# Kernel optimization log

Measured on AMD Instinct MI355X. Metric: run time of the kernel, lower is better.

The kernel has to match this reference:

```python
import jax, jax.numpy as jnp
import numpy as np

N_NODES = 100000
N_EDGES = 1600000
IN_DIM = 32
OUT_DIM = 64


def setup_inputs() -> dict:
    key = jax.random.key(0)
    k1, k2, k3, k4, k5 = jax.random.split(key, 5)
    feature = jax.random.normal(k1, (N_NODES, IN_DIM), dtype=jnp.float32)
    src = jax.random.randint(k2, (N_EDGES,), 0, N_NODES, dtype=jnp.int32)
    dst = jax.random.randint(k3, (N_EDGES,), 0, N_NODES, dtype=jnp.int32)
    W = jax.random.normal(k4, (IN_DIM, OUT_DIM), dtype=jnp.float32) * (1.0 / np.sqrt(IN_DIM))
    b = jax.random.normal(k5, (OUT_DIM,), dtype=jnp.float32) * 0.01
    return {"feature": feature, "src": src, "dst": dst, "W": W, "b": b}


def reference(feature, src, dst, W, b):
    # copy_u + sum: gather source features along edges, segment-sum into dst nodes
    msgs = feature[src]  # [E, in_dim]
    h_neigh = jax.ops.segment_sum(msgs, dst, num_segments=N_NODES)  # [N, in_dim]
    # linear projection
    return h_neigh @ W + b  # [N, out_dim]
```

## Files before the change

### kernel.cpp

```cpp
#include <hip/hip_runtime.h>

#define IN_DIM 32
#define OUT_DIM 64
#define NB_SCAN 391

__global__ __launch_bounds__(256) void hist_kernel(
    const int* __restrict__ dst, int* __restrict__ counts, int n_edges) {
    int e = blockIdx.x * 256 + threadIdx.x;
    if (e < n_edges) atomicAdd(&counts[dst[e]], 1);
}

__global__ __launch_bounds__(256) void scan1_kernel(
    const int* __restrict__ counts, int* __restrict__ row_start,
    int* __restrict__ block_sums, int n) {
    __shared__ int tmp[256];
    int tx = threadIdx.x;
    int idx = blockIdx.x * 256 + tx;
    int v = (idx < n) ? counts[idx] : 0;
    tmp[tx] = v;
    __syncthreads();
    for (int off = 1; off < 256; off <<= 1) {
        int t = (tx >= off) ? tmp[tx - off] : 0;
        __syncthreads();
        tmp[tx] += t;
        __syncthreads();
    }
    if (idx < n) row_start[idx] = tmp[tx] - v;
    if (tx == 255) block_sums[blockIdx.x] = tmp[255];
}

__global__ __launch_bounds__(512) void scan2_kernel(int* __restrict__ block_sums, int nb) {
    __shared__ int tmp[512];
    int tx = threadIdx.x;
    int v = (tx < nb) ? block_sums[tx] : 0;
    tmp[tx] = v;
    __syncthreads();
    for (int off = 1; off < 512; off <<= 1) {
        int t = (tx >= off) ? tmp[tx - off] : 0;
        __syncthreads();
        tmp[tx] += t;
        __syncthreads();
    }
    if (tx < nb) block_sums[tx] = tmp[tx] - v;
}

__global__ __launch_bounds__(256) void finalize_kernel(
    int* __restrict__ row_start, const int* __restrict__ block_sums,
    int* __restrict__ cursor, int n, int n_edges) {
    int idx = blockIdx.x * 256 + threadIdx.x;
    if (idx < n) {
        int v = row_start[idx] + block_sums[blockIdx.x];
        row_start[idx] = v;
        cursor[idx] = v;
    }
    if (blockIdx.x == 0 && threadIdx.x == 0) row_start[n] = n_edges;
}

__global__ __launch_bounds__(256) void scatter_kernel(
    const int* __restrict__ src, const int* __restrict__ dst,
    int* __restrict__ cursor, int* __restrict__ edge_src, int n_edges) {
    int e = blockIdx.x * 256 + threadIdx.x;
    if (e < n_edges) {
        int pos = atomicAdd(&cursor[dst[e]], 1);
        edge_src[pos] = src[e];
    }
}

__global__ __launch_bounds__(256) void gather_proj_kernel(
    const float* __restrict__ feature, const int* __restrict__ row_start,
    const int* __restrict__ edge_src, const float* __restrict__ W,
    const float* __restrict__ b, float* __restrict__ out, int n_nodes) {
    __shared__ float Ws[IN_DIM * OUT_DIM];
    __shared__ float bs[OUT_DIM];
    __shared__ float hs[8][IN_DIM];
    int tx = threadIdx.x;

    for (int i = tx; i < IN_DIM * OUT_DIM; i += 256) Ws[i] = W[i];
    if (tx < OUT_DIM) bs[tx] = b[tx];

    int slot = tx >> 5, lane = tx & 31;
    int node = blockIdx.x * 8 + slot;
    float acc = 0.0f;
    if (node < n_nodes) {
        int s0 = row_start[node], s1 = row_start[node + 1];
        int i = s0;
        for (; i + 4 <= s1; i += 4) {
            int ea = edge_src[i], eb = edge_src[i + 1];
            int ec = edge_src[i + 2], ed = edge_src[i + 3];
            float fa = feature[(long long)ea * IN_DIM + lane];
            float fb = feature[(long long)eb * IN_DIM + lane];
            float fc = feature[(long long)ec * IN_DIM + lane];
            float fd = feature[(long long)ed * IN_DIM + lane];
            acc += fa + fb + fc + fd;
        }
        for (; i < s1; ++i) acc += feature[(long long)edge_src[i] * IN_DIM + lane];
    }
    hs[slot][lane] = acc;
    __syncthreads();

    int node0 = blockIdx.x * 8;
#pragma unroll
    for (int it = 0; it < 2; ++it) {
        int idx = tx + it * 256;
        int sl = idx >> 6, col = idx & 63;
        int n2 = node0 + sl;
        if (n2 >= n_nodes) continue;
        float a = bs[col];
#pragma unroll
        for (int k = 0; k < IN_DIM; ++k) a += hs[sl][k] * Ws[k * OUT_DIM + col];
        out[(long long)n2 * OUT_DIM + col] = a;
    }
}

extern "C" void kernel_launch(void* const* d_in, const int* in_sizes, int n_in,
                              void* d_out, int out_size, void* d_ws, size_t ws_size,
                              hipStream_t stream) {
    const float* feature = (const float*)d_in[0];
    const int* src = (const int*)d_in[1];
    const int* dst = (const int*)d_in[2];
    const float* W = (const float*)d_in[3];
    const float* b = (const float*)d_in[4];
    float* out = (float*)d_out;

    int n_nodes = in_sizes[0] / IN_DIM;
    int n_edges = in_sizes[1];

    int* counts = (int*)d_ws;
    int* row_start = counts + n_nodes;
    int* cursor = row_start + n_nodes + 1;
    int* block_sums = cursor + n_nodes;
    int* edge_src = block_sums + 512;

    (void)hipMemsetAsync(counts, 0, (size_t)n_nodes * sizeof(int), stream);

    int eb = (n_edges + 255) / 256;
    int nb = (n_nodes + 255) / 256;
    hist_kernel<<<eb, 256, 0, stream>>>(dst, counts, n_edges);
    scan1_kernel<<<nb, 256, 0, stream>>>(counts, row_start, block_sums, n_nodes);
    scan2_kernel<<<1, 512, 0, stream>>>(block_sums, nb);
    finalize_kernel<<<nb, 256, 0, stream>>>(row_start, block_sums, cursor, n_nodes, n_edges);
    scatter_kernel<<<eb, 256, 0, stream>>>(src, dst, cursor, edge_src, n_edges);

    int gblocks = (n_nodes + 7) / 8;
    gather_proj_kernel<<<gblocks, 256, 0, stream>>>(feature, row_start, edge_src, W, b, out, n_nodes);
}
```

Measured before the change: 324.6 us.

## Replace per-node CSR build with bucketed counting sort and shared-memory aggregation

Edges are sorted into 256-node buckets rather than per-node CSR. Histogram and reorder use block-local shared-memory atomics, and each block writes its own per-bucket counts. Each aggregation block accumulates its bucket's node features in shared memory with shared atomics, then applies the projection. This removes the global atomics on 100k counters and the memset, at the cost of fewer, larger aggregation blocks and shared-atomic contention.

After: 477.5 us. 47.1% more time.

```diff
diff --git a/kernel.cpp b/kernel.cpp
--- a/kernel.cpp
+++ b/kernel.cpp
@@ -2,16 +2,30 @@
 
 #define IN_DIM 32
 #define OUT_DIM 64
-#define NB_SCAN 391
+#define BUCKET_SHIFT 8
+#define NODES_PER_BUCKET 256
+#define NBUCK_MAX 512
+#define EPB 8192
 
-__global__ __launch_bounds__(256) void hist_kernel(
-    const int* __restrict__ dst, int* __restrict__ counts, int n_edges) {
-    int e = blockIdx.x * 256 + threadIdx.x;
-    if (e < n_edges) atomicAdd(&counts[dst[e]], 1);
+__global__ __launch_bounds__(512) void hist_kernel(
+    const int* __restrict__ dst, int* __restrict__ counts,
+    int n_edges, int nb1, int nbuck) {
+    __shared__ int hist[NBUCK_MAX];
+    int tx = threadIdx.x;
+    for (int i = tx; i < nbuck; i += 512) hist[i] = 0;
+    __syncthreads();
+    int base = blockIdx.x * EPB;
+#pragma unroll
+    for (int j = 0; j < EPB / 512; ++j) {
+        int e = base + j * 512 + tx;
+        if (e < n_edges) atomicAdd(&hist[dst[e] >> BUCKET_SHIFT], 1);
+    }
+    __syncthreads();
+    for (int i = tx; i < nbuck; i += 512) counts[i * nb1 + blockIdx.x] = hist[i];
 }
 
 __global__ __launch_bounds__(256) void scan1_kernel(
-    const int* __restrict__ counts, int* __restrict__ row_start,
+    const int* __restrict__ counts, int* __restrict__ offsets,
     int* __restrict__ block_sums, int n) {
     __shared__ int tmp[256];
     int tx = threadIdx.x;
@@ -25,7 +39,7 @@
         tmp[tx] += t;
         __syncthreads();
     }
-    if (idx < n) row_start[idx] = tmp[tx] - v;
+    if (idx < n) offsets[idx] = tmp[tx] - v;
     if (tx == 255) block_sums[blockIdx.x] = tmp[255];
 }
 
@@ -45,70 +59,74 @@
 }
 
 __global__ __launch_bounds__(256) void finalize_kernel(
-    int* __restrict__ row_start, const int* __restrict__ block_sums,
-    int* __restrict__ cursor, int n, int n_edges) {
+    int* __restrict__ offsets, const int* __restrict__ block_sums, int n) {
     int idx = blockIdx.x * 256 + threadIdx.x;
-    if (idx < n) {
-        int v = row_start[idx] + block_sums[blockIdx.x];
-        row_start[idx] = v;
-        cursor[idx] = v;
-    }
-    if (blockIdx.x == 0 && threadIdx.x == 0) row_start[n] = n_edges;
+    if (idx < n) offsets[idx] += block_sums[blockIdx.x];
 }
 
-__global__ __launch_bounds__(256) void scatter_kernel(
+__global__ __launch_bounds__(512) void reorder_kernel(
     const int* __restrict__ src, const int* __restrict__ dst,
-    int* __restrict__ cursor, int* __restrict__ edge_src, int n_edges) {
-    int e = blockIdx.x * 256 + threadIdx.x;
-    if (e < n_edges) {
-        int pos = atomicAdd(&cursor[dst[e]], 1);
-        edge_src[pos] = src[e];
+    const int* __restrict__ offsets, int* __restrict__ rec,
+    int n_edges, int nb1, int nbuck) {
+    __shared__ int cur[NBUCK_MAX];
+    int tx = threadIdx.x;
+    for (int i = tx; i < nbuck; i += 512) cur[i] = offsets[i * nb1 + blockIdx.x];
+    __syncthreads();
+    int base = blockIdx.x * EPB;
+#pragma unroll
+    for (int j = 0; j < EPB / 512; ++j) {
+        int e = base + j * 512 + tx;
+        if (e < n_edges) {
+            int d = dst[e];
+            int pos = atomicAdd(&cur[d >> BUCKET_SHIFT], 1);
+            rec[pos] = (src[e] << BUCKET_SHIFT) | (d & (NODES_PER_BUCKET - 1));
+        }
     }
 }
 
-__global__ __launch_bounds__(256) void gather_proj_kernel(
-    const float* __restrict__ feature, const int* __restrict__ row_start,
-    const int* __restrict__ edge_src, const float* __restrict__ W,
-    const float* __restrict__ b, float* __restrict__ out, int n_nodes) {
+__global__ __launch_bounds__(512) void aggproj_kernel(
+    const float* __restrict__ feature, const int* __restrict__ offsets,
+    const int* __restrict__ rec, const float* __restrict__ W,
+    const float* __restrict__ b, float* __restrict__ out,
+    int n_nodes, int n_edges, int nb1, int nbuck) {
+    __shared__ float h[NODES_PER_BUCKET * IN_DIM];
     __shared__ float Ws[IN_DIM * OUT_DIM];
     __shared__ float bs[OUT_DIM];
-    __shared__ float hs[8][IN_DIM];
     int tx = threadIdx.x;
+    int bk = blockIdx.x;
 
-    for (int i = tx; i < IN_DIM * OUT_DIM; i += 256) Ws[i] = W[i];
+    for (int i = tx; i < NODES_PER_BUCKET * IN_DIM; i += 512) h[i] = 0.0f;
+    for (int i = tx; i < IN_DIM * OUT_DIM; i += 512) Ws[i] = W[i];
     if (tx < OUT_DIM) bs[tx] = b[tx];
 
-    int slot = tx >> 5, lane = tx & 31;
-    int node = blockIdx.x * 8 + slot;
-    float acc = 0.0f;
-    if (node < n_nodes) {
-        int s0 = row_start[node], s1 = row_start[node + 1];
-        int i = s0;
-        for (; i + 4 <= s1; i += 4) {
-            int ea = edge_src[i], eb = edge_src[i + 1];
-            int ec = edge_src[i + 2], ed = edge_src[i + 3];
-            float fa = feature[(long long)ea * IN_DIM + lane];
-            float fb = feature[(long long)eb * IN_DIM + lane];
-            float fc = feature[(long long)ec * IN_DIM + lane];
-            float fd = feature[(long long)ed * IN_DIM + lane];
-            acc += fa + fb + fc + fd;
-        }
-        for (; i < s1; ++i) acc += feature[(long long)edge_src[i] * IN_DIM + lane];
-    }
-    hs[slot][lane] = acc;
+    int start = offsets[bk * nb1];
+    int end = (bk + 1 < nbuck) ? offsets[(bk + 1) * nb1] : n_edges;
     __syncthreads();
 
-    int node0 = blockIdx.x * 8;
+    int grp = tx >> 5, lane = tx & 31;
+    for (int e0 = start + grp * 8; e0 < end; e0 += 16 * 8) {
 #pragma unroll
-    for (int it = 0; it < 2; ++it) {
-        int idx = tx + it * 256;
-        int sl = idx >> 6, col = idx & 63;
-        int n2 = node0 + sl;
-        if (n2 >= n_nodes) continue;
-        float a = bs[col];
+        for (int j = 0; j < 8; ++j) {
+            int e = e0 + j;
+            int r = (e < end) ? rec[e] : 0;
+            float v = (e < end) ? feature[(long long)(r >> BUCKET_SHIFT) * IN_DIM + lane] : 0.0f;
+            atomicAdd(&h[(r & (NODES_PER_BUCKET - 1)) * IN_DIM + lane], v);
+        }
+    }
+    __syncthreads();
+
+    int node0 = bk * NODES_PER_BUCKET;
 #pragma unroll
-        for (int k = 0; k < IN_DIM; ++k) a += hs[sl][k] * Ws[k * OUT_DIM + col];
-        out[(long long)n2 * OUT_DIM + col] = a;
+    for (int it = 0; it < NODES_PER_BUCKET * OUT_DIM / 512; ++it) {
+        int idx = it * 512 + tx;
+        int col = idx & 63, nl = idx >> 6;
+        int node = node0 + nl;
+        if (node >= n_nodes) break;
+        float acc = bs[col];
+#pragma unroll
+        for (int k = 0; k < IN_DIM; ++k)
+            acc += h[nl * IN_DIM + k] * Ws[k * OUT_DIM + col];
+        out[(long long)node * OUT_DIM + col] = acc;
     }
 }
 
@@ -125,22 +143,21 @@
     int n_nodes = in_sizes[0] / IN_DIM;
     int n_edges = in_sizes[1];
 
+    int nb1 = (n_edges + EPB - 1) / EPB;
+    int nbuck = (n_nodes + NODES_PER_BUCKET - 1) / NODES_PER_BUCKET;
+    int ncounts = nbuck * nb1;
+
     int* counts = (int*)d_ws;
-    int* row_start = counts + n_nodes;
-    int* cursor = row_start + n_nodes + 1;
-    int* block_sums = cursor + n_nodes;
-    int* edge_src = block_sums + 512;
+    int* offsets = counts + ncounts;
+    int* block_sums = offsets + ncounts;
+    int* rec = block_sums + 512;
 
-    (void)hipMemsetAsync(counts, 0, (size_t)n_nodes * sizeof(int), stream);
-
-    int eb = (n_edges + 255) / 256;
-    int nb = (n_nodes + 255) / 256;
-    hist_kernel<<<eb, 256, 0, stream>>>(dst, counts, n_edges);
-    scan1_kernel<<<nb, 256, 0, stream>>>(counts, row_start, block_sums, n_nodes);
-    scan2_kernel<<<1, 512, 0, stream>>>(block_sums, nb);
-    finalize_kernel<<<nb, 256, 0, stream>>>(row_start, block_sums, cursor, n_nodes, n_edges);
-    scatter_kernel<<<eb, 256, 0, stream>>>(src, dst, cursor, edge_src, n_edges);
-
-    int gblocks = (n_nodes + 7) / 8;
-    gather_proj_kernel<<<gblocks, 256, 0, stream>>>(feature, row_start, edge_src, W, b, out, n_nodes);
+    hist_kernel<<<nb1, 512, 0, stream>>>(dst, counts, n_edges, nb1, nbuck);
+    int sb = (ncounts + 255) / 256;
+    scan1_kernel<<<sb, 256, 0, stream>>>(counts, offsets, block_sums, ncounts);
+    scan2_kernel<<<1, 512, 0, stream>>>(block_sums, sb);
+    finalize_kernel<<<sb, 256, 0, stream>>>(offsets, block_sums, ncounts);
+    reorder_kernel<<<nb1, 512, 0, stream>>>(src, dst, offsets, rec, n_edges, nb1, nbuck);
+    aggproj_kernel<<<nbuck, 512, 0, stream>>>(feature, offsets, rec, W, b, out,
+                                              n_nodes, n_edges, nb1, nbuck);
 }
```
